# Kernel tuning notes

Hardware: AMD Instinct MI355X
Metric: run time of the kernel (lower is better)

Reference implementation:

```python
import jax, jax.numpy as jnp
import numpy as np

WEIGHT_BIT = 8
ACT_BIT = 8
EPS = 1e-8

def ste_round(v):
    # straight-through estimator round (matches torch ste_round in QAT)
    return v + jax.lax.stop_gradient(jnp.round(v) - v)

def setup_inputs() -> dict:
    key = jax.random.key(0)
    k1, k2, k3, k4 = jax.random.split(key, 4)
    B, D_IN, D_OUT = 8192, 4096, 4096
    x = jax.random.normal(k1, (B, D_IN), dtype=jnp.float32)
    act_scaling_factor = jax.random.uniform(k2, (1,), dtype=jnp.float32, minval=0.01, maxval=0.05)
    W = jax.random.normal(k3, (D_OUT, D_IN), dtype=jnp.float32) * 0.02
    b = jax.random.normal(k4, (D_OUT,), dtype=jnp.float32) * 0.02
    return {"x": x, "act_scaling_factor": act_scaling_factor, "W": W, "b": b}

def reference(x, act_scaling_factor, W, b):
    n_w = 2 ** (WEIGHT_BIT - 1) - 1  # 127
    # ---- QuantLinear: symmetric per-channel weight quantization ----
    w_absmax = jnp.maximum(jnp.abs(W.min(axis=1)), jnp.abs(W.max(axis=1)))  # [out]
    fc_sf = jnp.maximum(w_absmax, EPS) / n_w  # weight scaling factor, [out]
    w_int = jnp.clip(ste_round(W / fc_sf[:, None]), -n_w - 1, n_w)
    bias_sf = fc_sf * act_scaling_factor  # [out] (act_sf is scalar-shaped [1])
    b_int = ste_round(b / bias_sf)
    x_int = x / act_scaling_factor
    out = (jnp.matmul(x_int, w_int.T) + b_int) * bias_sf  # [B, out]
    # ---- ReLU ----
    out = jax.nn.relu(out)
    # ---- QuantAct, asymmetric per-tensor requantization ----
    levels = 2 ** ACT_BIT - 1  # 255
    x_min = jnp.minimum(out.min(), 0.0)
    x_max = jnp.maximum(out.max(), 0.0)
    act_sf_new = jnp.maximum(x_max - x_min, EPS) / levels  # scalar
    zp = jnp.round(-x_min / act_sf_new)
    x_q = jnp.clip(ste_round(out / act_sf_new) + zp, 0.0, float(levels))
    x_out = (x_q - zp) * act_sf_new
    return (x_out, fc_sf, jnp.reshape(act_sf_new, (1,)))
```

## Files before the change

### kernel.cpp

```cpp
#include <hip/hip_runtime.h>
#include <hip/hip_bf16.h>
#include <stdint.h>

#define B_DIM 8192
#define IN_DIM 4096
#define OUT_DIM 4096

typedef __attribute__((ext_vector_type(8))) short s16x8;
typedef __attribute__((ext_vector_type(4))) float f32x4;

__device__ __forceinline__ unsigned short f2bf_rn(float f) {
    unsigned int u = __float_as_uint(f);
    u = (u + 0x7FFFu + ((u >> 16) & 1u)) >> 16;
    return (unsigned short)u;
}

__device__ __forceinline__ void async16(unsigned short* l, const unsigned short* g) {
    __builtin_amdgcn_global_load_lds(
        (const __attribute__((address_space(1))) void*)g,
        (__attribute__((address_space(3))) void*)l, 16, 0, 0);
}

__global__ __launch_bounds__(256) void prep(
    const float* __restrict__ W, const float* __restrict__ b,
    const float* __restrict__ act_sf, const float* __restrict__ x,
    unsigned short* __restrict__ wq, unsigned short* __restrict__ xq,
    float* __restrict__ fc_sf_out, float* __restrict__ bb,
    float* __restrict__ gmax)
{
    __shared__ float red[4];
    int t = threadIdx.x;
    if (blockIdx.x < OUT_DIM) {
        int o = blockIdx.x;
        const float4* Wr = (const float4*)(W + (size_t)o * IN_DIM);
        float4 v[4];
        float amax = 0.f;
#pragma unroll
        for (int j = 0; j < 4; ++j) {
            v[j] = Wr[t + j * 256];
            amax = fmaxf(amax, fmaxf(fmaxf(fabsf(v[j].x), fabsf(v[j].y)),
                                     fmaxf(fabsf(v[j].z), fabsf(v[j].w))));
        }
#pragma unroll
        for (int off = 32; off > 0; off >>= 1)
            amax = fmaxf(amax, __shfl_down(amax, off, 64));
        if ((t & 63) == 0) red[t >> 6] = amax;
        __syncthreads();
        float wmax = fmaxf(fmaxf(red[0], red[1]), fmaxf(red[2], red[3]));
        float sf = fmaxf(wmax, 1e-8f) / 127.0f;

        unsigned short* wr = wq + (size_t)o * IN_DIM;
#pragma unroll
        for (int j = 0; j < 4; ++j) {
            ushort4 q;
            q.x = f2bf_rn(fminf(fmaxf(rintf(v[j].x / sf), -128.f), 127.f));
            q.y = f2bf_rn(fminf(fmaxf(rintf(v[j].y / sf), -128.f), 127.f));
            q.z = f2bf_rn(fminf(fmaxf(rintf(v[j].z / sf), -128.f), 127.f));
            q.w = f2bf_rn(fminf(fmaxf(rintf(v[j].w / sf), -128.f), 127.f));
            ((ushort4*)wr)[t + j * 256] = q;
        }
        if (t == 0) {
            fc_sf_out[o] = sf;
            float bsf = sf * act_sf[0];
            float bi = rintf(b[o] / bsf);
            bb[o] = bi * bsf;
            if (o == 0) gmax[0] = 0.f;
        }
    } else {
        size_t i = ((size_t)(blockIdx.x - OUT_DIM) * 256 + t) * 8;
#pragma unroll
        for (int j = 0; j < 2; ++j) {
            float4 v = *(const float4*)(x + i + j * 4);
            ushort4 q;
            q.x = f2bf_rn(v.x); q.y = f2bf_rn(v.y);
            q.z = f2bf_rn(v.z); q.w = f2bf_rn(v.w);
            *(ushort4*)(xq + i + j * 4) = q;
        }
    }
}

__global__ __launch_bounds__(256) void gemm_bt(
    const unsigned short* __restrict__ A, const unsigned short* __restrict__ Bw,
    const float* __restrict__ fc_sf, const float* __restrict__ bb,
    float* __restrict__ C, float* __restrict__ gmax)
{
    __shared__ unsigned short sA[128 * 64];
    __shared__ unsigned short sB[128 * 64];
    __shared__ float redm[4];

    int t = threadIdx.x;
    int bn = blockIdx.x & 31;
    int bm = blockIdx.x >> 5;
    int lane = t & 63;
    int w = t >> 6;
    int quad = lane >> 4;
    int l16 = lane & 15;
    int m0 = bm * 128, n0 = bn * 128;
    int wm = (w & 1) * 64, wn = (w >> 1) * 64;

    int r0 = t >> 3;
    int gc = (t & 7) ^ (r0 & 7);
    const unsigned short* gA[4];
    const unsigned short* gB[4];
    unsigned short* lA[4];
    unsigned short* lB[4];
#pragma unroll
    for (int j = 0; j < 4; ++j) {
        gA[j] = A + (size_t)(m0 + j * 32 + r0) * IN_DIM + gc * 8;
        gB[j] = Bw + (size_t)(n0 + j * 32 + r0) * IN_DIM + gc * 8;
        lA[j] = sA + (j * 256 + t) * 8;
        lB[j] = sB + (j * 256 + t) * 8;
    }

    int swzl = l16 & 7;
    const unsigned short* pa[2];
    const unsigned short* pb[2];
#pragma unroll
    for (int h = 0; h < 2; ++h) {
        pa[h] = sA + (wm + l16) * 64 + ((4 * h + quad) ^ swzl) * 8;
        pb[h] = sB + (wn + l16) * 64 + ((4 * h + quad) ^ swzl) * 8;
    }

    f32x4 acc[4][4];
#pragma unroll
    for (int mi = 0; mi < 4; ++mi)
#pragma unroll
        for (int ni = 0; ni < 4; ++ni)
            acc[mi][ni] = (f32x4){0.f, 0.f, 0.f, 0.f};

    for (int kk = 0; kk < IN_DIM; kk += 64) {
        __syncthreads();
#pragma unroll
        for (int j = 0; j < 4; ++j) {
            async16(lA[j], gA[j] + kk);
            async16(lB[j], gB[j] + kk);
        }
        asm volatile("s_waitcnt vmcnt(0)" ::: "memory");
        __syncthreads();

#pragma unroll
        for (int h = 0; h < 2; ++h) {
            s16x8 af[4], bf[4];
#pragma unroll
            for (int i = 0; i < 4; ++i) af[i] = *(const s16x8*)(pa[h] + i * 16 * 64);
#pragma unroll
            for (int i = 0; i < 4; ++i) bf[i] = *(const s16x8*)(pb[h] + i * 16 * 64);
#pragma unroll
            for (int mi = 0; mi < 4; ++mi)
#pragma unroll
                for (int ni = 0; ni < 4; ++ni)
                    acc[mi][ni] = __builtin_amdgcn_mfma_f32_16x16x32_bf16(
                        af[mi], bf[ni], acc[mi][ni], 0, 0, 0);
        }
    }

    float tmax = 0.f;
#pragma unroll
    for (int ni = 0; ni < 4; ++ni) {
        int col = n0 + wn + ni * 16 + l16;
        float s = fc_sf[col];
        float bbv = bb[col];
#pragma unroll
        for (int mi = 0; mi < 4; ++mi) {
            int rowb = m0 + wm + mi * 16 + quad * 4;
#pragma unroll
            for (int r = 0; r < 4; ++r) {
                float vv = acc[mi][ni][r] * s + bbv;
                vv = fmaxf(vv, 0.f);
                tmax = fmaxf(tmax, vv);
                C[(size_t)(rowb + r) * OUT_DIM + col] = vv;
            }
        }
    }
#pragma unroll
    for (int off = 32; off > 0; off >>= 1)
        tmax = fmaxf(tmax, __shfl_down(tmax, off, 64));
    if (lane == 0) redm[w] = tmax;
    __syncthreads();
    if (t == 0) {
        float bmax = fmaxf(fmaxf(redm[0], redm[1]), fmaxf(redm[2], redm[3]));
        atomicMax((int*)gmax, __float_as_int(bmax));
    }
}

__global__ __launch_bounds__(256) void requant(float* __restrict__ C,
    const float* __restrict__ gmax, float* __restrict__ sf_out)
{
    float sf = fmaxf(gmax[0], 1e-8f) / 255.0f;
    size_t i = ((size_t)blockIdx.x * 256 + threadIdx.x) * 16;
#pragma unroll
    for (int j = 0; j < 4; ++j) {
        float4 v = *(const float4*)(C + i + j * 4);
        v.x = fminf(rintf(v.x / sf), 255.f) * sf;
        v.y = fminf(rintf(v.y / sf), 255.f) * sf;
        v.z = fminf(rintf(v.z / sf), 255.f) * sf;
        v.w = fminf(rintf(v.w / sf), 255.f) * sf;
        *(float4*)(C + i + j * 4) = v;
    }
    if (i == 0) sf_out[0] = sf;
}

extern "C" void kernel_launch(void* const* d_in, const int* in_sizes, int n_in,
                              void* d_out, int out_size, void* d_ws, size_t ws_size,
                              hipStream_t stream)
{
    const float* x      = (const float*)d_in[0];
    const float* act_sf = (const float*)d_in[1];
    const float* W      = (const float*)d_in[2];
    const float* b      = (const float*)d_in[3];

    float* out        = (float*)d_out;
    float* fc_sf_out  = out + (size_t)B_DIM * OUT_DIM;
    float* act_sf_out = fc_sf_out + OUT_DIM;

    char* ws = (char*)d_ws;
    float* bb   = (float*)ws;
    float* gmax = (float*)(ws + 16384);
    unsigned short* xq = (unsigned short*)(ws + 32768);
    unsigned short* wq = xq + (size_t)B_DIM * IN_DIM;

    prep<<<OUT_DIM + (B_DIM * IN_DIM) / 2048, 256, 0, stream>>>(
        W, b, act_sf, x, wq, xq, fc_sf_out, bb, gmax);
    gemm_bt<<<(B_DIM / 128) * (OUT_DIM / 128), 256, 0, stream>>>(
        xq, wq, fc_sf_out, bb, out, gmax);
    requant<<<(B_DIM * OUT_DIM) / 4096, 256, 0, stream>>>(out, gmax, act_sf_out);
}
```

Baseline: 632.2 us.

## Stage GEMM epilogue through LDS for coalesced stores, emit bf16 intermediate

The GEMM epilogue now applies scale, bias and ReLU in registers, then stages each half-tile through shared memory. Each thread writes contiguous 128-byte row segments, replacing the strided per-element stores. When workspace allows, the intermediate is stored as bf16 in scratch and the requant kernel expands it to fp32 for the final output, roughly halving intermediate write and read traffic. This adds two extra barriers, and bf16 rounding of the pre-requant values may shift a few quantization bins.

```diff
diff --git a/kernel.cpp b/kernel.cpp
--- a/kernel.cpp
+++ b/kernel.cpp
@@ -79,14 +79,17 @@
     }
 }
 
+template <bool CB16>
 __global__ __launch_bounds__(256) void gemm_bt(
     const unsigned short* __restrict__ A, const unsigned short* __restrict__ Bw,
     const float* __restrict__ fc_sf, const float* __restrict__ bb,
-    float* __restrict__ C, float* __restrict__ gmax)
+    void* __restrict__ Cout, float* __restrict__ gmax)
 {
-    __shared__ unsigned short sA[128 * 64];
-    __shared__ unsigned short sB[128 * 64];
-    __shared__ float redm[4];
+    __shared__ __align__(16) unsigned char smem[33296];
+    unsigned short* sA = (unsigned short*)smem;
+    unsigned short* sB = (unsigned short*)(smem + 16384);
+    float* stage = (float*)smem;
+    float* redm  = (float*)(smem + 33280);
 
     int t = threadIdx.x;
     int bn = blockIdx.x & 31;
@@ -154,48 +157,108 @@
         }
     }
 
-    float tmax = 0.f;
+    float sc[4], bv[4];
 #pragma unroll
     for (int ni = 0; ni < 4; ++ni) {
         int col = n0 + wn + ni * 16 + l16;
-        float s = fc_sf[col];
-        float bbv = bb[col];
-#pragma unroll
-        for (int mi = 0; mi < 4; ++mi) {
-            int rowb = m0 + wm + mi * 16 + quad * 4;
+        sc[ni] = fc_sf[col];
+        bv[ni] = bb[col];
+    }
+    float tmax = 0.f;
+#pragma unroll
+    for (int mi = 0; mi < 4; ++mi)
+#pragma unroll
+        for (int ni = 0; ni < 4; ++ni)
 #pragma unroll
             for (int r = 0; r < 4; ++r) {
-                float vv = acc[mi][ni][r] * s + bbv;
-                vv = fmaxf(vv, 0.f);
+                float vv = fmaxf(acc[mi][ni][r] * sc[ni] + bv[ni], 0.f);
+                acc[mi][ni][r] = vv;
                 tmax = fmaxf(tmax, vv);
-                C[(size_t)(rowb + r) * OUT_DIM + col] = vv;
             }
-        }
-    }
 #pragma unroll
     for (int off = 32; off > 0; off >>= 1)
         tmax = fmaxf(tmax, __shfl_down(tmax, off, 64));
     if (lane == 0) redm[w] = tmax;
-    __syncthreads();
+
+#pragma unroll
+    for (int p = 0; p < 2; ++p) {
+        __syncthreads();
+        if ((w & 1) == p) {
+#pragma unroll
+            for (int mi = 0; mi < 4; ++mi)
+#pragma unroll
+                for (int ni = 0; ni < 4; ++ni)
+#pragma unroll
+                    for (int r = 0; r < 4; ++r) {
+                        int lrow = mi * 16 + quad * 4 + r;
+                        stage[lrow * 130 + wn + ni * 16 + l16] = acc[mi][ni][r];
+                    }
+        }
+        __syncthreads();
+        int row = t >> 2;
+        int cc = (t & 3) * 32;
+        const float* src = stage + row * 130 + cc;
+        size_t gbase = (size_t)(m0 + p * 64 + row) * OUT_DIM + n0 + cc;
+        if (CB16) {
+            unsigned short* dst = (unsigned short*)Cout + gbase;
+#pragma unroll
+            for (int j = 0; j < 4; ++j) {
+                float4 v0 = *(const float4*)(src + j * 8);
+                float4 v1 = *(const float4*)(src + j * 8 + 4);
+                s16x8 q;
+                q[0] = (short)f2bf_rn(v0.x); q[1] = (short)f2bf_rn(v0.y);
+                q[2] = (short)f2bf_rn(v0.z); q[3] = (short)f2bf_rn(v0.w);
+                q[4] = (short)f2bf_rn(v1.x); q[5] = (short)f2bf_rn(v1.y);
+                q[6] = (short)f2bf_rn(v1.z); q[7] = (short)f2bf_rn(v1.w);
+                *(s16x8*)(dst + j * 8) = q;
+            }
+        } else {
+            float* dst = (float*)Cout + gbase;
+#pragma unroll
+            for (int j = 0; j < 8; ++j)
+                *(float4*)(dst + j * 4) = *(const float4*)(src + j * 4);
+        }
+    }
     if (t == 0) {
         float bmax = fmaxf(fmaxf(redm[0], redm[1]), fmaxf(redm[2], redm[3]));
         atomicMax((int*)gmax, __float_as_int(bmax));
     }
 }
 
-__global__ __launch_bounds__(256) void requant(float* __restrict__ C,
-    const float* __restrict__ gmax, float* __restrict__ sf_out)
+template <bool CB16>
+__global__ __launch_bounds__(256) void requant(const void* __restrict__ Cin,
+    float* __restrict__ out, const float* __restrict__ gmax,
+    float* __restrict__ sf_out)
 {
     float sf = fmaxf(gmax[0], 1e-8f) / 255.0f;
     size_t i = ((size_t)blockIdx.x * 256 + threadIdx.x) * 16;
-#pragma unroll
-    for (int j = 0; j < 4; ++j) {
-        float4 v = *(const float4*)(C + i + j * 4);
-        v.x = fminf(rintf(v.x / sf), 255.f) * sf;
-        v.y = fminf(rintf(v.y / sf), 255.f) * sf;
-        v.z = fminf(rintf(v.z / sf), 255.f) * sf;
-        v.w = fminf(rintf(v.w / sf), 255.f) * sf;
-        *(float4*)(C + i + j * 4) = v;
+    if (CB16) {
+        const unsigned short* cq = (const unsigned short*)Cin + i;
+#pragma unroll
+        for (int j = 0; j < 4; ++j) {
+            ushort4 q = *(const ushort4*)(cq + j * 4);
+            float4 v;
+            v.x = __uint_as_float((unsigned)q.x << 16);
+            v.y = __uint_as_float((unsigned)q.y << 16);
+            v.z = __uint_as_float((unsigned)q.z << 16);
+            v.w = __uint_as_float((unsigned)q.w << 16);
+            v.x = fminf(rintf(v.x / sf), 255.f) * sf;
+            v.y = fminf(rintf(v.y / sf), 255.f) * sf;
+            v.z = fminf(rintf(v.z / sf), 255.f) * sf;
+            v.w = fminf(rintf(v.w / sf), 255.f) * sf;
+            *(float4*)(out + i + j * 4) = v;
+        }
+    } else {
+        float* C = out;
+#pragma unroll
+        for (int j = 0; j < 4; ++j) {
+            float4 v = *(const float4*)(C + i + j * 4);
+            v.x = fminf(rintf(v.x / sf), 255.f) * sf;
+            v.y = fminf(rintf(v.y / sf), 255.f) * sf;
+            v.z = fminf(rintf(v.z / sf), 255.f) * sf;
+            v.w = fminf(rintf(v.w / sf), 255.f) * sf;
+            *(float4*)(C + i + j * 4) = v;
+        }
     }
     if (i == 0) sf_out[0] = sf;
 }
@@ -218,10 +281,25 @@
     float* gmax = (float*)(ws + 16384);
     unsigned short* xq = (unsigned short*)(ws + 32768);
     unsigned short* wq = xq + (size_t)B_DIM * IN_DIM;
+    unsigned short* cq = wq + (size_t)OUT_DIM * IN_DIM;
+
+    size_t need = 32768 + ((size_t)B_DIM * IN_DIM + (size_t)OUT_DIM * IN_DIM
+                           + (size_t)B_DIM * OUT_DIM) * 2;
 
     prep<<<OUT_DIM + (B_DIM * IN_DIM) / 2048, 256, 0, stream>>>(
         W, b, act_sf, x, wq, xq, fc_sf_out, bb, gmax);
-    gemm_bt<<<(B_DIM / 128) * (OUT_DIM / 128), 256, 0, stream>>>(
-        xq, wq, fc_sf_out, bb, out, gmax);
-    requant<<<(B_DIM * OUT_DIM) / 4096, 256, 0, stream>>>(out, gmax, act_sf_out);
-}
+
+    int gemm_grid = (B_DIM / 128) * (OUT_DIM / 128);
+    int rq_grid = (B_DIM * OUT_DIM) / 4096;
+    if (ws_size >= need) {
+        gemm_bt<true><<<gemm_grid, 256, 0, stream>>>(
+            xq, wq, fc_sf_out, bb, (void*)cq, gmax);
+        requant<true><<<rq_grid, 256, 0, stream>>>(
+            (const void*)cq, out, gmax, act_sf_out);
+    } else {
+        gemm_bt<false><<<gemm_grid, 256, 0, stream>>>(
+            xq, wq, fc_sf_out, bb, (void*)out, gmax);
+        requant<false><<<rq_grid, 256, 0, stream>>>(
+            (const void*)out, out, gmax, act_sf_out);
+    }
+}
```

New measurement: 619.8 us. No clear change (-2.0%).
